# Performance work log

Measured on AMD Instinct MI355X. Metric: run time of the kernel, lower is better.

Reference implementation:

```python
import jax, jax.numpy as jnp
import numpy as np

N_NODES = 10000
N_EDGES = 640000
HIDDEN = 128
OUT = 10

def setup_inputs() -> dict:
    key = jax.random.key(0)
    k1, k2, k3, k4 = jax.random.split(key, 4)
    x = jax.random.normal(k1, (N_NODES, HIDDEN), dtype=jnp.float32)
    edge_index = jax.random.randint(k2, (2, N_EDGES), 0, N_NODES, dtype=jnp.int64)
    # ClassifierMLP2 params: Linear(2*hidden -> hidden) -> ReLU -> Linear(hidden -> out)
    W1 = jax.random.normal(k3, (2 * HIDDEN, HIDDEN), dtype=jnp.float32) / np.sqrt(2 * HIDDEN)
    b1 = jnp.zeros((HIDDEN,), dtype=jnp.float32)
    W2 = jax.random.normal(k4, (HIDDEN, OUT), dtype=jnp.float32) / np.sqrt(HIDDEN)
    b2 = jnp.zeros((OUT,), dtype=jnp.float32)
    return {"x": x, "edge_index": edge_index, "W1": W1, "b1": b1, "W2": W2, "b2": b2}

def reference(x, edge_index, W1, b1, W2, b2):
    # mix_node_features(..., node_feat_mixing='cat'): gather src/dst node
    # embeddings per edge and concatenate along feature dim -> [E, 2*H]
    src, dst = edge_index[0], edge_index[1]
    edges_x = jnp.concatenate([x[src], x[dst]], axis=-1)  # [E, 2H]
    # ClassifierMLP2 (dropout inactive at inference)
    h = jax.nn.relu(edges_x @ W1 + b1)                    # [E, H]
    return h @ W2 + b2                                    # [E, OUT]
```

## Files before the change

### kernel.cpp

```cpp
#include <hip/hip_runtime.h>


typedef _Float16 f16;
typedef _Float16 f16x8 __attribute__((ext_vector_type(8)));
typedef float    f32x4 __attribute__((ext_vector_type(4)));

#define HID  128
#define TWOH 256
#define OUTD 10

__global__ __launch_bounds__(256) void prep_weights(
    const float* __restrict__ W1,
    const float* __restrict__ W2,
    f16* __restrict__ W1P,
    f16* __restrict__ W2P)
{
    const int slot = blockIdx.x * 256 + threadIdx.x;
    if (slot < 4096) {
        const int lane = slot & 63, i = slot >> 6;
        const int r = lane & 15, g = lane >> 4;
        const int wv = i >> 4, ct = (i >> 2) & 3, st = i & 3;
        const int c = wv * 64 + ct * 16 + r;
        f16x8 v;
#pragma unroll
        for (int j = 0; j < 8; ++j) {
            const int k = st * 32 + g * 8 + j;
            const float w = (c < HID) ? W1[k * HID + c]
                                      : W1[(HID + k) * HID + (c - HID)];
            v[j] = (f16)w;
        }
        *(f16x8*)(W1P + (long)slot * 8) = v;
    } else if (slot < 4096 + 256) {
        const int s2 = slot - 4096;
        const int lane = s2 & 63, st = s2 >> 6;
        const int r = lane & 15, g = lane >> 4;
        f16x8 v;
#pragma unroll
        for (int j = 0; j < 8; ++j)
            v[j] = (r < OUTD) ? (f16)W2[(st * 32 + g * 8 + j) * OUTD + r] : (f16)0.f;
        *(f16x8*)(W2P + (long)s2 * 8) = v;
    }
}

__global__ __launch_bounds__(256, 3) void node_AB(
    const float* __restrict__ x,
    const f16* __restrict__ W1P,
    const float* __restrict__ b1,
    f16* __restrict__ AB,
    int n_nodes)
{
    const int t = threadIdx.x;
    const int lane = t & 63;
    const int r = lane & 15, g = lane >> 4;
    const int wv = t >> 6;
    const int n0 = blockIdx.x * 16;

    const int xrow = (n0 + r < n_nodes) ? (n0 + r) : (n_nodes - 1);
    float4 xl[4][2];
#pragma unroll
    for (int st = 0; st < 4; ++st) {
        const float* xp = x + (long)xrow * HID + st * 32 + g * 8;
        xl[st][0] = *(const float4*)xp;
        xl[st][1] = *(const float4*)(xp + 4);
    }

    f16x8 w1f[4][4];
    float bias[4];
#pragma unroll
    for (int ct = 0; ct < 4; ++ct) {
        const int c = wv * 64 + ct * 16 + r;
        bias[ct] = (c < HID) ? b1[c] : 0.f;
#pragma unroll
        for (int st = 0; st < 4; ++st)
            w1f[ct][st] = *(const f16x8*)(W1P + ((long)((wv * 16 + ct * 4 + st)) * 64 + lane) * 8);
    }

    f32x4 acc[4] = {{0,0,0,0},{0,0,0,0},{0,0,0,0},{0,0,0,0}};
#pragma unroll
    for (int st = 0; st < 4; ++st) {
        f16x8 a;
        a[0] = (f16)xl[st][0].x; a[1] = (f16)xl[st][0].y;
        a[2] = (f16)xl[st][0].z; a[3] = (f16)xl[st][0].w;
        a[4] = (f16)xl[st][1].x; a[5] = (f16)xl[st][1].y;
        a[6] = (f16)xl[st][1].z; a[7] = (f16)xl[st][1].w;
#pragma unroll
        for (int ct = 0; ct < 4; ++ct)
            acc[ct] = __builtin_amdgcn_mfma_f32_16x16x32_f16(a, w1f[ct][st], acc[ct], 0, 0, 0);
    }

#pragma unroll
    for (int ct = 0; ct < 4; ++ct) {
        const int c = wv * 64 + ct * 16 + r;
#pragma unroll
        for (int q = 0; q < 4; ++q) {
            const int node = n0 + g * 4 + q;
            if (node < n_nodes)
                AB[(long)node * TWOH + c] = (f16)(acc[ct][q] + bias[ct]);
        }
    }
}

__global__ __launch_bounds__(256, 3) void edge_mlp(
    const f16* __restrict__ AB,
    const int* __restrict__ ei,
    const f16* __restrict__ W2P,
    const float* __restrict__ b2,
    float* __restrict__ out,
    int n_edges)
{
    __shared__ float stage[4][160];
    const int t = threadIdx.x;
    const int lane = t & 63;
    const int r = lane & 15, g = lane >> 4;
    const int wv = t >> 6;

    f16x8 w2f[4];
#pragma unroll
    for (int st = 0; st < 4; ++st)
        w2f[st] = *(const f16x8*)(W2P + ((long)st * 64 + lane) * 8);
    const float bj = b2[(r < OUTD) ? r : 0];

    const long eb = (long)blockIdx.x * 512 + wv * 128;

    int sn[8], dn[8];
#pragma unroll
    for (int it = 0; it < 8; ++it) {
        const long e = eb + it * 16 + r;
        const long ec = (e < n_edges) ? e : (n_edges - 1);
        sn[it] = ei[ec];
        dn[it] = ei[(long)n_edges + ec];
    }

    const f16x8 zt = {0, 0, 0, 0, 0, 0, 0, 0};

    if (eb + 128 <= n_edges) {
        asm volatile("" ::
            "v"(w2f[0]), "v"(w2f[1]), "v"(w2f[2]), "v"(w2f[3]), "v"(bj),
            "v"(sn[0]), "v"(sn[1]), "v"(sn[2]), "v"(sn[3]),
            "v"(sn[4]), "v"(sn[5]), "v"(sn[6]), "v"(sn[7]),
            "v"(dn[0]), "v"(dn[1]), "v"(dn[2]), "v"(dn[3]),
            "v"(dn[4]), "v"(dn[5]), "v"(dn[6]), "v"(dn[7]));

#define DECL(IT) f16x8 pa##IT##0, pa##IT##1, pa##IT##2, pa##IT##3, \
                       pc##IT##0, pc##IT##1, pc##IT##2, pc##IT##3;
        DECL(0) DECL(1) DECL(2) DECL(3) DECL(4) DECL(5) DECL(6) DECL(7)

#define ISSUE(IT) { \
    const f16* _pa = AB + ((long)sn[IT] * TWOH + g * 8); \
    const f16* _pb = AB + ((long)dn[IT] * TWOH + HID + g * 8); \
    asm volatile("global_load_dwordx4 %0, %1, off"            : "=v"(pa##IT##0) : "v"(_pa)); \
    asm volatile("global_load_dwordx4 %0, %1, off offset:64"  : "=v"(pa##IT##1) : "v"(_pa)); \
    asm volatile("global_load_dwordx4 %0, %1, off offset:128" : "=v"(pa##IT##2) : "v"(_pa)); \
    asm volatile("global_load_dwordx4 %0, %1, off offset:192" : "=v"(pa##IT##3) : "v"(_pa)); \
    asm volatile("global_load_dwordx4 %0, %1, off"            : "=v"(pc##IT##0) : "v"(_pb)); \
    asm volatile("global_load_dwordx4 %0, %1, off offset:64"  : "=v"(pc##IT##1) : "v"(_pb)); \
    asm volatile("global_load_dwordx4 %0, %1, off offset:128" : "=v"(pc##IT##2) : "v"(_pb)); \
    asm volatile("global_load_dwordx4 %0, %1, off offset:192" : "=v"(pc##IT##3) : "v"(_pb)); \
}

#define WAITN(IT, NSTR) \
    asm volatile("s_waitcnt vmcnt(" NSTR ")" \
        : "+v"(pa##IT##0), "+v"(pa##IT##1), "+v"(pa##IT##2), "+v"(pa##IT##3), \
          "+v"(pc##IT##0), "+v"(pc##IT##1), "+v"(pc##IT##2), "+v"(pc##IT##3)); \
    __builtin_amdgcn_sched_barrier(0);

#define COMPUTE(IT) { \
    f32x4 acc = {0, 0, 0, 0}; \
    f16x8 s; \
    s = __builtin_elementwise_max(pa##IT##0 + pc##IT##0, zt); \
    acc = __builtin_amdgcn_mfma_f32_16x16x32_f16(s, w2f[0], acc, 0, 0, 0); \
    s = __builtin_elementwise_max(pa##IT##1 + pc##IT##1, zt); \
    acc = __builtin_amdgcn_mfma_f32_16x16x32_f16(s, w2f[1], acc, 0, 0, 0); \
    s = __builtin_elementwise_max(pa##IT##2 + pc##IT##2, zt); \
    acc = __builtin_amdgcn_mfma_f32_16x16x32_f16(s, w2f[2], acc, 0, 0, 0); \
    s = __builtin_elementwise_max(pa##IT##3 + pc##IT##3, zt); \
    acc = __builtin_amdgcn_mfma_f32_16x16x32_f16(s, w2f[3], acc, 0, 0, 0); \
    if (r < OUTD) { \
        _Pragma("unroll") \
        for (int q = 0; q < 4; ++q) \
            stage[wv][(g * 4 + q) * OUTD + r] = acc[q] + bj; \
    } \
    __builtin_amdgcn_wave_barrier(); \
    if (lane < 40) { \
        const f32x4 vv = *(const f32x4*)&stage[wv][lane * 4]; \
        float* po = out + (eb + IT * 16) * OUTD + lane * 4; \
        asm volatile("global_store_dwordx4 %0, %1, off" :: "v"(po), "v"(vv) : "memory"); \
    } \
    __builtin_amdgcn_wave_barrier(); \
}

        ISSUE(0) ISSUE(1) ISSUE(2)
        WAITN(0, "16") COMPUTE(0) ISSUE(3)
        WAITN(1, "17") COMPUTE(1) ISSUE(4)
        WAITN(2, "18") COMPUTE(2) ISSUE(5)
        WAITN(3, "18") COMPUTE(3) ISSUE(6)
        WAITN(4, "18") COMPUTE(4) ISSUE(7)
        WAITN(5, "18") COMPUTE(5)
        WAITN(6, "10") COMPUTE(6)
        WAITN(7, "2")  COMPUTE(7)
        asm volatile("s_waitcnt vmcnt(0)");
#undef DECL
#undef ISSUE
#undef WAITN
#undef COMPUTE
    } else {
#pragma unroll
        for (int it = 0; it < 8; ++it) {
            f32x4 acc = {0, 0, 0, 0};
#pragma unroll
            for (int st = 0; st < 4; ++st) {
                const f16x8 a = *(const f16x8*)(AB + ((long)sn[it] * TWOH + st * 32 + g * 8));
                const f16x8 c = *(const f16x8*)(AB + ((long)dn[it] * TWOH + HID + st * 32 + g * 8));
                const f16x8 s = __builtin_elementwise_max(a + c, zt);
                acc = __builtin_amdgcn_mfma_f32_16x16x32_f16(s, w2f[st], acc, 0, 0, 0);
            }
            if (r < OUTD) {
#pragma unroll
                for (int q = 0; q < 4; ++q) {
                    const long ee = eb + it * 16 + g * 4 + q;
                    if (ee < n_edges) out[ee * OUTD + r] = acc[q] + bj;
                }
            }
        }
    }
}

extern "C" void kernel_launch(void* const* d_in, const int* in_sizes, int n_in,
                              void* d_out, int out_size, void* d_ws, size_t ws_size,
                              hipStream_t stream) {
    const float* x  = (const float*)d_in[0];
    const int*   ei = (const int*)d_in[1];
    const float* W1 = (const float*)d_in[2];
    const float* b1 = (const float*)d_in[3];
    const float* W2 = (const float*)d_in[4];
    const float* b2 = (const float*)d_in[5];
    float* out = (float*)d_out;

    const int n_nodes = in_sizes[0] / HID;
    const int n_edges = in_sizes[1] / 2;

    f16* AB  = (f16*)d_ws;
    f16* W1P = AB + (long)n_nodes * TWOH;
    f16* W2P = W1P + 4096 * 8;

    prep_weights<<<17, 256, 0, stream>>>(W1, W2, W1P, W2P);

    node_AB<<<(n_nodes + 15) / 16, 256, 0, stream>>>(x, W1P, b1, AB, n_nodes);

    edge_mlp<<<(n_edges + 511) / 512, 256, 0, stream>>>(AB, ei, W2P, b2, out, n_edges);
}
```

Baseline: 60.35 us.

## Split node_AB columns across blocks, halve edges per wave, drop LDS output staging

```diff
diff --git a/kernel.cpp b/kernel.cpp
--- a/kernel.cpp
+++ b/kernel.cpp
@@ -19,8 +19,8 @@
     if (slot < 4096) {
         const int lane = slot & 63, i = slot >> 6;
         const int r = lane & 15, g = lane >> 4;
-        const int wv = i >> 4, ct = (i >> 2) & 3, st = i & 3;
-        const int c = wv * 64 + ct * 16 + r;
+        const int T = i >> 2, st = i & 3;
+        const int c = T * 16 + r;
         f16x8 v;
 #pragma unroll
         for (int j = 0; j < 8; ++j) {
@@ -53,7 +53,8 @@
     const int lane = t & 63;
     const int r = lane & 15, g = lane >> 4;
     const int wv = t >> 6;
-    const int n0 = blockIdx.x * 16;
+    const int n0 = (blockIdx.x >> 1) * 16;
+    const int ch = blockIdx.x & 1;
 
     const int xrow = (n0 + r < n_nodes) ? (n0 + r) : (n_nodes - 1);
     float4 xl[4][2];
@@ -64,18 +65,21 @@
         xl[st][1] = *(const float4*)(xp + 4);
     }
 
-    f16x8 w1f[4][4];
-    float bias[4];
-#pragma unroll
-    for (int ct = 0; ct < 4; ++ct) {
-        const int c = wv * 64 + ct * 16 + r;
+    f16x8 w1f[2][4];
+    float bias[2];
+    int cc[2];
+#pragma unroll
+    for (int ct = 0; ct < 2; ++ct) {
+        const int T = ch * 8 + wv * 2 + ct;
+        const int c = T * 16 + r;
+        cc[ct] = c;
         bias[ct] = (c < HID) ? b1[c] : 0.f;
 #pragma unroll
         for (int st = 0; st < 4; ++st)
-            w1f[ct][st] = *(const f16x8*)(W1P + ((long)((wv * 16 + ct * 4 + st)) * 64 + lane) * 8);
-    }
-
-    f32x4 acc[4] = {{0,0,0,0},{0,0,0,0},{0,0,0,0},{0,0,0,0}};
+            w1f[ct][st] = *(const f16x8*)(W1P + ((long)(T * 4 + st) * 64 + lane) * 8);
+    }
+
+    f32x4 acc[2] = {{0,0,0,0},{0,0,0,0}};
 #pragma unroll
     for (int st = 0; st < 4; ++st) {
         f16x8 a;
@@ -84,18 +88,17 @@
         a[4] = (f16)xl[st][1].x; a[5] = (f16)xl[st][1].y;
         a[6] = (f16)xl[st][1].z; a[7] = (f16)xl[st][1].w;
 #pragma unroll
-        for (int ct = 0; ct < 4; ++ct)
+        for (int ct = 0; ct < 2; ++ct)
             acc[ct] = __builtin_amdgcn_mfma_f32_16x16x32_f16(a, w1f[ct][st], acc[ct], 0, 0, 0);
     }
 
 #pragma unroll
-    for (int ct = 0; ct < 4; ++ct) {
-        const int c = wv * 64 + ct * 16 + r;
+    for (int ct = 0; ct < 2; ++ct) {
 #pragma unroll
         for (int q = 0; q < 4; ++q) {
             const int node = n0 + g * 4 + q;
             if (node < n_nodes)
-                AB[(long)node * TWOH + c] = (f16)(acc[ct][q] + bias[ct]);
+                AB[(long)node * TWOH + cc[ct]] = (f16)(acc[ct][q] + bias[ct]);
         }
     }
 }
@@ -108,7 +111,6 @@
     float* __restrict__ out,
     int n_edges)
 {
-    __shared__ float stage[4][160];
     const int t = threadIdx.x;
     const int lane = t & 63;
     const int r = lane & 15, g = lane >> 4;
@@ -120,11 +122,11 @@
         w2f[st] = *(const f16x8*)(W2P + ((long)st * 64 + lane) * 8);
     const float bj = b2[(r < OUTD) ? r : 0];
 
-    const long eb = (long)blockIdx.x * 512 + wv * 128;
-
-    int sn[8], dn[8];
-#pragma unroll
-    for (int it = 0; it < 8; ++it) {
+    const long eb = (long)blockIdx.x * 256 + wv * 64;
+
+    int sn[4], dn[4];
+#pragma unroll
+    for (int it = 0; it < 4; ++it) {
         const long e = eb + it * 16 + r;
         const long ec = (e < n_edges) ? e : (n_edges - 1);
         sn[it] = ei[ec];
@@ -133,17 +135,16 @@
 
     const f16x8 zt = {0, 0, 0, 0, 0, 0, 0, 0};
 
-    if (eb + 128 <= n_edges) {
+    if (eb + 64 <= n_edges) {
         asm volatile("" ::
             "v"(w2f[0]), "v"(w2f[1]), "v"(w2f[2]), "v"(w2f[3]), "v"(bj),
             "v"(sn[0]), "v"(sn[1]), "v"(sn[2]), "v"(sn[3]),
-            "v"(sn[4]), "v"(sn[5]), "v"(sn[6]), "v"(sn[7]),
-            "v"(dn[0]), "v"(dn[1]), "v"(dn[2]), "v"(dn[3]),
-            "v"(dn[4]), "v"(dn[5]), "v"(dn[6]), "v"(dn[7]));
+            "v"(dn[0]), "v"(dn[1]), "v"(dn[2]), "v"(dn[3]));
 
 #define DECL(IT) f16x8 pa##IT##0, pa##IT##1, pa##IT##2, pa##IT##3, \
-                       pc##IT##0, pc##IT##1, pc##IT##2, pc##IT##3;
-        DECL(0) DECL(1) DECL(2) DECL(3) DECL(4) DECL(5) DECL(6) DECL(7)
+                       pc##IT##0, pc##IT##1, pc##IT##2, pc##IT##3; \
+                 f32x4 acc##IT = {0, 0, 0, 0};
+        DECL(0) DECL(1) DECL(2) DECL(3)
 
 #define ISSUE(IT) { \
     const f16* _pa = AB + ((long)sn[IT] * TWOH + g * 8); \
@@ -165,47 +166,39 @@
     __builtin_amdgcn_sched_barrier(0);
 
 #define COMPUTE(IT) { \
-    f32x4 acc = {0, 0, 0, 0}; \
     f16x8 s; \
     s = __builtin_elementwise_max(pa##IT##0 + pc##IT##0, zt); \
-    acc = __builtin_amdgcn_mfma_f32_16x16x32_f16(s, w2f[0], acc, 0, 0, 0); \
+    acc##IT = __builtin_amdgcn_mfma_f32_16x16x32_f16(s, w2f[0], acc##IT, 0, 0, 0); \
     s = __builtin_elementwise_max(pa##IT##1 + pc##IT##1, zt); \
-    acc = __builtin_amdgcn_mfma_f32_16x16x32_f16(s, w2f[1], acc, 0, 0, 0); \
+    acc##IT = __builtin_amdgcn_mfma_f32_16x16x32_f16(s, w2f[1], acc##IT, 0, 0, 0); \
     s = __builtin_elementwise_max(pa##IT##2 + pc##IT##2, zt); \
-    acc = __builtin_amdgcn_mfma_f32_16x16x32_f16(s, w2f[2], acc, 0, 0, 0); \
+    acc##IT = __builtin_amdgcn_mfma_f32_16x16x32_f16(s, w2f[2], acc##IT, 0, 0, 0); \
     s = __builtin_elementwise_max(pa##IT##3 + pc##IT##3, zt); \
-    acc = __builtin_amdgcn_mfma_f32_16x16x32_f16(s, w2f[3], acc, 0, 0, 0); \
-    if (r < OUTD) { \
-        _Pragma("unroll") \
-        for (int q = 0; q < 4; ++q) \
-            stage[wv][(g * 4 + q) * OUTD + r] = acc[q] + bj; \
-    } \
-    __builtin_amdgcn_wave_barrier(); \
-    if (lane < 40) { \
-        const f32x4 vv = *(const f32x4*)&stage[wv][lane * 4]; \
-        float* po = out + (eb + IT * 16) * OUTD + lane * 4; \
-        asm volatile("global_store_dwordx4 %0, %1, off" :: "v"(po), "v"(vv) : "memory"); \
-    } \
-    __builtin_amdgcn_wave_barrier(); \
-}
-
-        ISSUE(0) ISSUE(1) ISSUE(2)
-        WAITN(0, "16") COMPUTE(0) ISSUE(3)
-        WAITN(1, "17") COMPUTE(1) ISSUE(4)
-        WAITN(2, "18") COMPUTE(2) ISSUE(5)
-        WAITN(3, "18") COMPUTE(3) ISSUE(6)
-        WAITN(4, "18") COMPUTE(4) ISSUE(7)
-        WAITN(5, "18") COMPUTE(5)
-        WAITN(6, "10") COMPUTE(6)
-        WAITN(7, "2")  COMPUTE(7)
-        asm volatile("s_waitcnt vmcnt(0)");
+    acc##IT = __builtin_amdgcn_mfma_f32_16x16x32_f16(s, w2f[3], acc##IT, 0, 0, 0); \
+}
+
+        ISSUE(0) ISSUE(1)
+        WAITN(0, "8") COMPUTE(0) ISSUE(2)
+        WAITN(1, "8") COMPUTE(1) ISSUE(3)
+        WAITN(2, "8") COMPUTE(2)
+        WAITN(3, "0") COMPUTE(3)
+
+        if (r < OUTD) {
+#pragma unroll
+            for (int q = 0; q < 4; ++q) {
+                out[(eb +      g * 4 + q) * OUTD + r] = acc0[q] + bj;
+                out[(eb + 16 + g * 4 + q) * OUTD + r] = acc1[q] + bj;
+                out[(eb + 32 + g * 4 + q) * OUTD + r] = acc2[q] + bj;
+                out[(eb + 48 + g * 4 + q) * OUTD + r] = acc3[q] + bj;
+            }
+        }
 #undef DECL
 #undef ISSUE
 #undef WAITN
 #undef COMPUTE
     } else {
 #pragma unroll
-        for (int it = 0; it < 8; ++it) {
+        for (int it = 0; it < 4; ++it) {
             f32x4 acc = {0, 0, 0, 0};
 #pragma unroll
             for (int st = 0; st < 4; ++st) {
@@ -245,7 +238,7 @@
 
     prep_weights<<<17, 256, 0, stream>>>(W1, W2, W1P, W2P);
 
-    node_AB<<<(n_nodes + 15) / 16, 256, 0, stream>>>(x, W1P, b1, AB, n_nodes);
-
-    edge_mlp<<<(n_edges + 511) / 512, 256, 0, stream>>>(AB, ei, W2P, b2, out, n_edges);
-}
+    node_AB<<<((n_nodes + 15) / 16) * 2, 256, 0, stream>>>(x, W1P, b1, AB, n_nodes);
+
+    edge_mlp<<<(n_edges + 255) / 256, 256, 0, stream>>>(AB, ei, W2P, b2, out, n_edges);
+}
```

After: 64.48 us. +6.8%, slower.
